# Performance work log

Measured on AMD Instinct MI355X. Metric: run time of the kernel, lower is better.

The kernel has to match this reference:

```python
import jax, jax.numpy as jnp
import numpy as np

B, T, E, H = 1, 2048, 2048, 32
D = E // H  # head_dim = 64


def alibi_bias(n_heads, t_q, t_k, dtype):
    # slopes: 2^(-8*(h+1)/n_heads) for power-of-two head counts
    slopes = jnp.power(2.0, -8.0 * jnp.arange(1, n_heads + 1, dtype=jnp.float32) / n_heads)
    i = jnp.arange(t_q)[:, None] + (t_k - t_q)  # absolute query positions
    j = jnp.arange(t_k)[None, :]
    rel = (j - i).astype(dtype)                 # [t_q, t_k], <=0 on/below diagonal
    return (slopes[:, None, None] * rel).astype(dtype)  # [H, t_q, t_k]


def setup_inputs() -> dict:
    key = jax.random.key(0)
    kx, kq, kk, kv, ko = jax.random.split(key, 5)
    s = E ** -0.5
    x = jax.random.normal(kx, (B, T, E), dtype=jnp.float32)
    Wq = jax.random.normal(kq, (E, E), dtype=jnp.float32) * s
    Wk = jax.random.normal(kk, (D, E), dtype=jnp.float32) * s
    Wv = jax.random.normal(kv, (D, E), dtype=jnp.float32) * s
    Wo = jax.random.normal(ko, (E, E), dtype=jnp.float32) * s
    # causal mask: True where attention is disallowed (j > i)
    attention_mask = jnp.triu(jnp.ones((T, T), dtype=bool), k=1)[None, None]  # [1,1,T,T]
    return {"x": x, "Wq": Wq, "Wk": Wk, "Wv": Wv, "Wo": Wo, "attention_mask": attention_mask}


def reference(x, Wq, Wk, Wv, Wo, attention_mask):
    b, t, _ = x.shape
    scale = D ** -0.5
    q = (x @ Wq.T).reshape(b, t, H, D).transpose(0, 2, 1, 3)  # [b,H,t,D]
    k = x @ Wk.T                                              # [b,t,D] (single KV head)
    v = x @ Wv.T                                              # [b,t,D]
    attn = jnp.einsum('bhtd,bsd->bhts', q * scale, k)         # [b,H,t,t]
    attn = attn + alibi_bias(H, t, t, attn.dtype)[None]
    attn = jnp.where(attention_mask, jnp.asarray(-10000.0, attn.dtype), attn)
    w = jax.nn.softmax(attn, axis=-1)
    out = jnp.einsum('bhts,bsd->bhtd', w, v)                  # [b,H,t,D]
    out = out.transpose(0, 2, 1, 3).reshape(b, t, E)
    return out @ Wo.T
```

## Files before the change

### kernel.cpp

```cpp
#include <hip/hip_runtime.h>
#include <stdint.h>

typedef __bf16 bf16;
typedef __bf16 bf16x4 __attribute__((ext_vector_type(4)));
typedef __bf16 bf16x8 __attribute__((ext_vector_type(8)));
typedef short short4v __attribute__((ext_vector_type(4)));
typedef float floatx4 __attribute__((ext_vector_type(4)));

#define MFMA32(a, b, c) __builtin_amdgcn_mfma_f32_16x16x32_bf16((a), (b), (c), 0, 0, 0)

__device__ __forceinline__ floatx4 mfma16(bf16x4 a, bf16x4 b, floatx4 c) {
  return __builtin_amdgcn_mfma_f32_16x16x16bf16_1k(
      __builtin_bit_cast(short4v, a), __builtin_bit_cast(short4v, b), c, 0, 0, 0);
}

__device__ __forceinline__ void gload16(const void* g, void* l) {
  __builtin_amdgcn_global_load_lds(
      (const __attribute__((address_space(1))) void*)g,
      (__attribute__((address_space(3))) void*)l, 16, 0, 0);
}

__device__ __forceinline__ bf16x8 load8(const float* p) {
  float4 lo = *(const float4*)p;
  float4 hi = *(const float4*)(p + 4);
  bf16x8 r;
  r[0] = (bf16)lo.x; r[1] = (bf16)lo.y; r[2] = (bf16)lo.z; r[3] = (bf16)lo.w;
  r[4] = (bf16)hi.x; r[5] = (bf16)hi.y; r[6] = (bf16)hi.z; r[7] = (bf16)hi.w;
  return r;
}

__global__ __launch_bounds__(256) void conv3(const float* __restrict__ a, bf16* __restrict__ ab,
                                             const float* __restrict__ b, bf16* __restrict__ bb,
                                             const float* __restrict__ c, bf16* __restrict__ cb) {
  const int i = blockIdx.x * 256 + threadIdx.x;
  const float* src = blockIdx.y == 0 ? a : (blockIdx.y == 1 ? b : c);
  bf16* dst = blockIdx.y == 0 ? ab : (blockIdx.y == 1 ? bb : cb);
  ((bf16x8*)dst)[i] = load8(src + (size_t)i * 8);
}

__global__ __launch_bounds__(256) void pack_kv(const float* __restrict__ Kf,
                                               const float* __restrict__ Vf,
                                               bf16* __restrict__ Kb,
                                               bf16* __restrict__ Vtb) {
  int i = blockIdx.x * 256 + threadIdx.x;
  if (i < 2048 * 64) {
    Kb[i] = (bf16)Kf[i];
    const int t = i >> 6, d = i & 63;
    Vtb[(size_t)d * 2048 + t] = (bf16)Vf[i];
  }
}

template <typename TC>
__global__ __launch_bounds__(256) void gemm_bt_a(const bf16* __restrict__ A,
                                                 const bf16* __restrict__ B,
                                                 TC* __restrict__ C,
                                                 int M, int N, int K) {
  __shared__ __align__(16) bf16 As[2][64 * 32];
  __shared__ __align__(16) bf16 Bs[2][128 * 32];
  const int tid = threadIdx.x;
  const int wave = tid >> 6, lane = tid & 63;
  const int quad = lane >> 4, l16 = lane & 15;
  const int m0 = blockIdx.y * 64, n0 = blockIdx.x * 128;
  const int wm = (wave >> 1) * 32, wn = (wave & 1) * 64;

  floatx4 acc[2][4];
#pragma unroll
  for (int i = 0; i < 2; i++)
#pragma unroll
    for (int j = 0; j < 4; j++) acc[i][j] = (floatx4)0.f;

  const int srow = tid >> 2, scol = (tid & 3) * 8;
  const bf16* Ap = A + (size_t)(m0 + srow) * K + scol;
  const bf16* Bp = B + (size_t)(n0 + srow) * K + scol;

  auto stage = [&](int k0, int buf) {
    gload16(Ap + k0, (char*)As[buf] + tid * 16);
    gload16(Bp + k0, (char*)Bs[buf] + tid * 16);
    gload16(Bp + (size_t)64 * K + k0, (char*)Bs[buf] + 4096 + tid * 16);
  };
  auto compute = [&](int buf) {
    bf16x8 af[2], bfr[4];
#pragma unroll
    for (int mt = 0; mt < 2; mt++)
      af[mt] = *(const bf16x8*)(&As[buf][(wm + mt * 16 + l16) * 32 + quad * 8]);
#pragma unroll
    for (int nt = 0; nt < 4; nt++)
      bfr[nt] = *(const bf16x8*)(&Bs[buf][(wn + nt * 16 + l16) * 32 + quad * 8]);
#pragma unroll
    for (int mt = 0; mt < 2; mt++)
#pragma unroll
      for (int nt = 0; nt < 4; nt++)
        acc[mt][nt] = MFMA32(af[mt], bfr[nt], acc[mt][nt]);
  };

  stage(0, 0);
  for (int k0 = 0; k0 < K; k0 += 64) {
    __syncthreads();
    if (k0 + 32 < K) stage(k0 + 32, 1);
    compute(0);
    __syncthreads();
    if (k0 + 64 < K) stage(k0 + 64, 0);
    compute(1);
  }

#pragma unroll
  for (int mt = 0; mt < 2; mt++) {
#pragma unroll
    for (int nt = 0; nt < 4; nt++) {
      const int col = n0 + wn + nt * 16 + l16;
      const int row = m0 + wm + mt * 16 + quad * 4;
#pragma unroll
      for (int r = 0; r < 4; r++)
        C[(size_t)(row + r) * N + col] = (TC)acc[mt][nt][r];
    }
  }
}

__global__ __launch_bounds__(256) void kv_gemm(const bf16* __restrict__ xb,
                                               const float* __restrict__ Wk,
                                               const float* __restrict__ Wv,
                                               float* __restrict__ Kf,
                                               float* __restrict__ Vf) {
  __shared__ __align__(16) bf16 As[128 * 40];
  __shared__ __align__(16) bf16 Bs[128 * 40];
  const int tid = threadIdx.x;
  const int wave = tid >> 6, lane = tid & 63;
  const int quad = lane >> 4, l16 = lane & 15;
  const int m0 = blockIdx.y * 128;
  const int kbeg = blockIdx.x * 256, kend = kbeg + 256;
  const int wm = (wave >> 1) * 64, wn = (wave & 1) * 64;

  floatx4 acc[4][4];
#pragma unroll
  for (int i = 0; i < 4; i++)
#pragma unroll
    for (int j = 0; j < 4; j++) acc[i][j] = (floatx4)0.f;

  const int sr = tid >> 2, sc = (tid & 3) * 8;

  for (int k0 = kbeg; k0 < kend; k0 += 32) {
    __syncthreads();
#pragma unroll
    for (int rr = 0; rr < 2; rr++) {
      const int row = sr + rr * 64;
      *(bf16x8*)(&As[row * 40 + sc]) =
          *(const bf16x8*)(&xb[(size_t)(m0 + row) * 2048 + k0 + sc]);
      const float* bsrc = (row < 64) ? &Wk[(size_t)row * 2048 + k0 + sc]
                                     : &Wv[(size_t)(row - 64) * 2048 + k0 + sc];
      *(bf16x8*)(&Bs[row * 40 + sc]) = load8(bsrc);
    }
    __syncthreads();

    bf16x8 af[4], bfr[4];
#pragma unroll
    for (int mt = 0; mt < 4; mt++)
      af[mt] = *(const bf16x8*)(&As[(wm + mt * 16 + l16) * 40 + quad * 8]);
#pragma unroll
    for (int nt = 0; nt < 4; nt++)
      bfr[nt] = *(const bf16x8*)(&Bs[(wn + nt * 16 + l16) * 40 + quad * 8]);
#pragma unroll
    for (int mt = 0; mt < 4; mt++)
#pragma unroll
      for (int nt = 0; nt < 4; nt++)
        acc[mt][nt] = MFMA32(af[mt], bfr[nt], acc[mt][nt]);
  }

#pragma unroll
  for (int mt = 0; mt < 4; mt++) {
#pragma unroll
    for (int nt = 0; nt < 4; nt++) {
      const int col = wn + nt * 16 + l16;
      const int row = m0 + wm + mt * 16 + quad * 4;
      float* dst = (col < 64) ? &Kf[(size_t)row * 64 + col]
                              : &Vf[(size_t)row * 64 + (col - 64)];
#pragma unroll
      for (int r = 0; r < 4; r++) atomicAdd(dst + (size_t)r * 64, acc[mt][nt][r]);
    }
  }
}

__global__ __launch_bounds__(512) void attn_kernel(const bf16* __restrict__ Q,
                                                   const bf16* __restrict__ Kb,
                                                   const bf16* __restrict__ Vtb,
                                                   bf16* __restrict__ O) {
  __shared__ __align__(16) bf16 Ks[2][64 * 72];
  __shared__ __align__(16) bf16 Vt[2][64 * 72];
  const int tid = threadIdx.x;
  const int wq = tid >> 6;
  const int lane = tid & 63;
  const int quad = lane >> 4, l16 = lane & 15;
  const int h = blockIdx.y;
  const int t = (blockIdx.y < 16) ? (15 - blockIdx.x) : blockIdx.x;
  const float scale2 = 0.125f * 1.44269504f;
  const float slope2 = exp2f(-0.25f * (float)(h + 1)) * 1.44269504f;

  float cq[4];
#pragma unroll
  for (int r = 0; r < 4; r++) cq[r] = slope2 * (float)(quad * 4 + r);
  const float s16 = slope2 * 16.f;
  const bf16x4 ones = {(bf16)1.f, (bf16)1.f, (bf16)1.f, (bf16)1.f};

  const int qi = t * 128 + wq * 16 + l16;
  bf16x8 qf[2];
#pragma unroll
  for (int kk = 0; kk < 2; kk++)
    qf[kk] = *(const bf16x8*)(&Q[(size_t)qi * 2048 + h * 64 + kk * 32 + quad * 8]);

  floatx4 oacc[4];
#pragma unroll
  for (int dt = 0; dt < 4; dt++) oacc[dt] = (floatx4)0.f;
  floatx4 lacc = (floatx4)0.f;

  const int r0 = tid >> 3, c0 = (tid & 7) * 8;
  const int ktmax = 2 * t + 1;
  const int qw0 = t * 128 + wq * 16;

  bf16x8 kreg = *(const bf16x8*)(&Kb[(size_t)r0 * 64 + c0]);
  bf16x8 vreg = *(const bf16x8*)(&Vtb[(size_t)r0 * 2048 + c0]);

  for (int kt = 0; kt <= ktmax; kt++) {
    const int buf = kt & 1;
    *(bf16x8*)(&Ks[buf][r0 * 72 + c0]) = kreg;
    *(bf16x8*)(&Vt[buf][r0 * 72 + c0]) = vreg;
    __syncthreads();
    if (kt < ktmax) {
      const int kn = (kt + 1) * 64;
      kreg = *(const bf16x8*)(&Kb[(size_t)(kn + r0) * 64 + c0]);
      vreg = *(const bf16x8*)(&Vtb[(size_t)r0 * 2048 + kn + c0]);
    }
    const int k0 = kt * 64;
    if (k0 > qw0 + 15) continue;

    floatx4 s[4];
#pragma unroll
    for (int mt = 0; mt < 4; mt++) s[mt] = (floatx4)0.f;
#pragma unroll
    for (int kk = 0; kk < 2; kk++) {
#pragma unroll
      for (int mt = 0; mt < 4; mt++) {
        bf16x8 kf = *(const bf16x8*)(&Ks[buf][(mt * 16 + l16) * 72 + kk * 32 + quad * 8]);
        s[mt] = MFMA32(kf, qf[kk], s[mt]);
      }
    }

    const float base0 = slope2 * (float)(k0 - qi);
    bf16x4 pb[4];
    if (k0 + 63 <= qw0) {
      float base = base0;
#pragma unroll
      for (int mt = 0; mt < 4; mt++) {
        bf16x4 tb;
#pragma unroll
        for (int r = 0; r < 4; r++)
          tb[r] = (bf16)exp2f(__builtin_fmaf(s[mt][r], scale2, base + cq[r]));
        pb[mt] = tb;
        base += s16;
      }
    } else {
      const int qloc = qi - k0;
      float base = base0;
#pragma unroll
      for (int mt = 0; mt < 4; mt++) {
        bf16x4 tb;
#pragma unroll
        for (int r = 0; r < 4; r++) {
          const int moff = mt * 16 + quad * 4 + r;
          const float p = exp2f(__builtin_fmaf(s[mt][r], scale2, base + cq[r]));
          tb[r] = (moff <= qloc) ? (bf16)p : (bf16)0.f;
        }
        pb[mt] = tb;
        base += s16;
      }
    }

#pragma unroll
    for (int mt = 0; mt < 4; mt++) {
      lacc = mfma16(ones, pb[mt], lacc);
#pragma unroll
      for (int dt = 0; dt < 4; dt++) {
        const bf16x4 va =
            *(const bf16x4*)(&Vt[buf][(dt * 16 + l16) * 72 + mt * 16 + quad * 4]);
        oacc[dt] = mfma16(va, pb[mt], oacc[dt]);
      }
    }
  }

  const float linv = 1.0f / lacc[0];
#pragma unroll
  for (int dt = 0; dt < 4; dt++) {
    bf16x4 ob;
#pragma unroll
    for (int r = 0; r < 4; r++) ob[r] = (bf16)(oacc[dt][r] * linv);
    *(bf16x4*)(&O[(size_t)qi * 2048 + h * 64 + dt * 16 + quad * 4]) = ob;
  }
}

extern "C" void kernel_launch(void* const* d_in, const int* in_sizes, int n_in,
                              void* d_out, int out_size, void* d_ws,
                              size_t ws_size, hipStream_t stream) {
  (void)in_sizes; (void)n_in; (void)out_size; (void)ws_size;
  const float* x = (const float*)d_in[0];
  const float* Wq = (const float*)d_in[1];
  const float* Wk = (const float*)d_in[2];
  const float* Wv = (const float*)d_in[3];
  const float* Wo = (const float*)d_in[4];
  float* out = (float*)d_out;

  const size_t NE = (size_t)2048 * 2048;
  bf16* xb = (bf16*)d_ws;
  bf16* Wqb = xb + NE;
  bf16* Wob = Wqb + NE;
  bf16* Qb = Wob + NE;
  float* Kf = (float*)(Qb + NE);
  float* Vf = Kf + 2048 * 64;
  bf16* Kb = (bf16*)(Vf + 2048 * 64);
  bf16* Vtb = Kb + 2048 * 64;
  bf16* AO = xb;

  hipMemsetAsync(Kf, 0, 2 * 2048 * 64 * sizeof(float), stream);
  conv3<<<dim3(2048, 3), 256, 0, stream>>>(x, xb, Wq, Wqb, Wo, Wob);
  gemm_bt_a<bf16><<<dim3(16, 32), 256, 0, stream>>>(xb, Wqb, Qb, 2048, 2048, 2048);
  kv_gemm<<<dim3(8, 16), 256, 0, stream>>>(xb, Wk, Wv, Kf, Vf);
  pack_kv<<<512, 256, 0, stream>>>(Kf, Vf, Kb, Vtb);
  attn_kernel<<<dim3(16, 32), 512, 0, stream>>>(Qb, Kb, Vtb, AO);
  gemm_bt_a<float><<<dim3(16, 32), 256, 0, stream>>>(AO, Wob, out, 2048, 2048, 2048);
}
```

Baseline: 241.3 us.

## Split attention key range across two wave groups, swizzle LDS, skip negligible ALiBi tiles

Doubles the attention block to 1024 threads, with two groups of waves each processing half of the key tiles for the same query rows. Partial outputs and row sums are combined through shared memory at the end. Key tiles whose ALiBi bias makes exp2 below 2^-44 are skipped, and the K/V shared-memory tiles use an XOR swizzle instead of padding. This aims to raise parallelism for long causal rows and cut wasted exp/MFMA work, at the cost of an extra reduction, higher LDS use and a small approximation.

```diff
diff --git a/kernel.cpp b/kernel.cpp
--- a/kernel.cpp
+++ b/kernel.cpp
@@ -179,14 +179,19 @@
   }
 }
 
-__global__ __launch_bounds__(512) void attn_kernel(const bf16* __restrict__ Q,
-                                                   const bf16* __restrict__ Kb,
-                                                   const bf16* __restrict__ Vtb,
-                                                   bf16* __restrict__ O) {
-  __shared__ __align__(16) bf16 Ks[2][64 * 72];
-  __shared__ __align__(16) bf16 Vt[2][64 * 72];
+__global__ __launch_bounds__(1024, 8) void attn_kernel(const bf16* __restrict__ Q,
+                                                       const bf16* __restrict__ Kb,
+                                                       const bf16* __restrict__ Vtb,
+                                                       bf16* __restrict__ O) {
+  __shared__ __align__(16) char smem[65536];
+  bf16* const Ksm = (bf16*)smem;
+  bf16* const Vsm = (bf16*)(smem + 32768);
+  float* const comb = (float*)smem;
+
   const int tid = threadIdx.x;
   const int wq = tid >> 6;
+  const int grp = wq >> 3;
+  const int wrow = wq & 7;
   const int lane = tid & 63;
   const int quad = lane >> 4, l16 = lane & 15;
   const int h = blockIdx.y;
@@ -200,7 +205,7 @@
   const float s16 = slope2 * 16.f;
   const bf16x4 ones = {(bf16)1.f, (bf16)1.f, (bf16)1.f, (bf16)1.f};
 
-  const int qi = t * 128 + wq * 16 + l16;
+  const int qi = t * 128 + wrow * 16 + l16;
   bf16x8 qf[2];
 #pragma unroll
   for (int kk = 0; kk < 2; kk++)
@@ -211,25 +216,41 @@
   for (int dt = 0; dt < 4; dt++) oacc[dt] = (floatx4)0.f;
   floatx4 lacc = (floatx4)0.f;
 
-  const int r0 = tid >> 3, c0 = (tid & 7) * 8;
-  const int ktmax = 2 * t + 1;
-  const int qw0 = t * 128 + wq * 16;
-
-  bf16x8 kreg = *(const bf16x8*)(&Kb[(size_t)r0 * 64 + c0]);
-  bf16x8 vreg = *(const bf16x8*)(&Vtb[(size_t)r0 * 2048 + c0]);
-
-  for (int kt = 0; kt <= ktmax; kt++) {
-    const int buf = kt & 1;
-    *(bf16x8*)(&Ks[buf][r0 * 72 + c0]) = kreg;
-    *(bf16x8*)(&Vt[buf][r0 * 72 + c0]) = vreg;
-    __syncthreads();
-    if (kt < ktmax) {
-      const int kn = (kt + 1) * 64;
-      kreg = *(const bf16x8*)(&Kb[(size_t)(kn + r0) * 64 + c0]);
-      vreg = *(const bf16x8*)(&Vtb[(size_t)r0 * 2048 + kn + c0]);
+  const int end = 2 * t + 2;
+  const int lo_key = t * 128 - (int)(44.f / slope2);
+  const int lo_t = (lo_key <= 0) ? 0 : (lo_key >> 6);
+  const int n = (end - lo_t + 1) >> 1;
+  const int base = lo_t + grp * n;
+  const int kt_last = end - 1;
+  const int qw0 = t * 128 + wrow * 16;
+
+  const int tg = tid & 511;
+  const int r0 = tg >> 3, sl = tg & 7;
+  const int wsw = ((sl ^ (r0 & 7)) << 3);
+  const int sx = l16 & 7;
+
+  int kn = min(base, kt_last) * 64;
+  bf16x8 kreg = *(const bf16x8*)(&Kb[(size_t)(kn + r0) * 64 + sl * 8]);
+  bf16x8 vreg = *(const bf16x8*)(&Vtb[(size_t)r0 * 2048 + kn + sl * 8]);
+
+  for (int i = 0; i < n; i++) {
+    const int kt = base + i;
+    const int bofs = (grp * 2 + (i & 1)) * 4096;
+    *(bf16x8*)(&Ksm[bofs + r0 * 64 + wsw]) = kreg;
+    *(bf16x8*)(&Vsm[bofs + r0 * 64 + wsw]) = vreg;
+    __syncthreads();
+    if (i + 1 < n) {
+      const int kn2 = min(kt + 1, kt_last) * 64;
+      kreg = *(const bf16x8*)(&Kb[(size_t)(kn2 + r0) * 64 + sl * 8]);
+      vreg = *(const bf16x8*)(&Vtb[(size_t)r0 * 2048 + kn2 + sl * 8]);
     }
     const int k0 = kt * 64;
+    if (kt >= end) continue;
     if (k0 > qw0 + 15) continue;
+    if ((float)(qw0 - k0 - 63) * slope2 > 44.f) continue;
+
+    const bf16* ks = Ksm + bofs;
+    const bf16* vs = Vsm + bofs;
 
     floatx4 s[4];
 #pragma unroll
@@ -238,7 +259,8 @@
     for (int kk = 0; kk < 2; kk++) {
 #pragma unroll
       for (int mt = 0; mt < 4; mt++) {
-        bf16x8 kf = *(const bf16x8*)(&Ks[buf][(mt * 16 + l16) * 72 + kk * 32 + quad * 8]);
+        bf16x8 kf = *(const bf16x8*)(
+            &ks[(mt * 16 + l16) * 64 + (((kk * 4 + quad) ^ sx) << 3)]);
         s[mt] = MFMA32(kf, qf[kk], s[mt]);
       }
     }
@@ -246,30 +268,30 @@
     const float base0 = slope2 * (float)(k0 - qi);
     bf16x4 pb[4];
     if (k0 + 63 <= qw0) {
-      float base = base0;
+      float b = base0;
 #pragma unroll
       for (int mt = 0; mt < 4; mt++) {
         bf16x4 tb;
 #pragma unroll
         for (int r = 0; r < 4; r++)
-          tb[r] = (bf16)exp2f(__builtin_fmaf(s[mt][r], scale2, base + cq[r]));
+          tb[r] = (bf16)exp2f(__builtin_fmaf(s[mt][r], scale2, b + cq[r]));
         pb[mt] = tb;
-        base += s16;
+        b += s16;
       }
     } else {
       const int qloc = qi - k0;
-      float base = base0;
+      float b = base0;
 #pragma unroll
       for (int mt = 0; mt < 4; mt++) {
         bf16x4 tb;
 #pragma unroll
         for (int r = 0; r < 4; r++) {
           const int moff = mt * 16 + quad * 4 + r;
-          const float p = exp2f(__builtin_fmaf(s[mt][r], scale2, base + cq[r]));
+          const float p = exp2f(__builtin_fmaf(s[mt][r], scale2, b + cq[r]));
           tb[r] = (moff <= qloc) ? (bf16)p : (bf16)0.f;
         }
         pb[mt] = tb;
-        base += s16;
+        b += s16;
       }
     }
 
@@ -278,20 +300,35 @@
       lacc = mfma16(ones, pb[mt], lacc);
 #pragma unroll
       for (int dt = 0; dt < 4; dt++) {
-        const bf16x4 va =
-            *(const bf16x4*)(&Vt[buf][(dt * 16 + l16) * 72 + mt * 16 + quad * 4]);
+        const int slot = 2 * mt + (quad >> 1);
+        const bf16x4 va = *(const bf16x4*)(
+            &vs[(dt * 16 + l16) * 64 + ((slot ^ sx) << 3) + (quad & 1) * 4]);
         oacc[dt] = mfma16(va, pb[mt], oacc[dt]);
       }
     }
   }
 
-  const float linv = 1.0f / lacc[0];
-#pragma unroll
-  for (int dt = 0; dt < 4; dt++) {
-    bf16x4 ob;
-#pragma unroll
-    for (int r = 0; r < 4; r++) ob[r] = (bf16)(oacc[dt][r] * linv);
-    *(bf16x4*)(&O[(size_t)qi * 2048 + h * 64 + dt * 16 + quad * 4]) = ob;
+  __syncthreads();
+  if (grp == 1) {
+    float* c = comb + (size_t)(wrow * 64 + lane) * 17;
+#pragma unroll
+    for (int dt = 0; dt < 4; dt++)
+#pragma unroll
+      for (int r = 0; r < 4; r++) c[dt * 4 + r] = oacc[dt][r];
+    c[16] = lacc[0];
+  }
+  __syncthreads();
+  if (grp == 0) {
+    const float* c = comb + (size_t)(wrow * 64 + lane) * 17;
+    const float linv = 1.0f / (lacc[0] + c[16]);
+#pragma unroll
+    for (int dt = 0; dt < 4; dt++) {
+      bf16x4 ob;
+#pragma unroll
+      for (int r = 0; r < 4; r++)
+        ob[r] = (bf16)((oacc[dt][r] + c[dt * 4 + r]) * linv);
+      *(bf16x4*)(&O[(size_t)qi * 2048 + h * 64 + dt * 16 + quad * 4]) = ob;
+    }
   }
 }
 
@@ -322,6 +359,6 @@
   gemm_bt_a<bf16><<<dim3(16, 32), 256, 0, stream>>>(xb, Wqb, Qb, 2048, 2048, 2048);
   kv_gemm<<<dim3(8, 16), 256, 0, stream>>>(xb, Wk, Wv, Kf, Vf);
   pack_kv<<<512, 256, 0, stream>>>(Kf, Vf, Kb, Vtb);
-  attn_kernel<<<dim3(16, 32), 512, 0, stream>>>(Qb, Kb, Vtb, AO);
+  attn_kernel<<<dim3(16, 32), 1024, 0, stream>>>(Qb, Kb, Vtb, AO);
   gemm_bt_a<float><<<dim3(16, 32), 256, 0, stream>>>(AO, Wob, out, 2048, 2048, 2048);
 }
```

New measurement: 300.0 us. 1.24x slower.
